# Optimization experiments

Hardware: AMD Instinct MI355X
Metric: run time of the kernel (lower is better)

Reference implementation:

```python
import jax, jax.numpy as jnp
import numpy as np

N_NODES = 100000
N_EDGES = 1600000
IN_F = 128
HID_F = 128
OUT_F = 128
HEAD_HID = 128
HEAD_OUT = 64


def setup_inputs() -> dict:
    key = jax.random.key(0)
    ks = jax.random.split(key, 16)
    glorot = lambda k, i, o: jax.random.normal(k, (i, o), jnp.float32) * (2.0 / (i + o)) ** 0.5
    return {
        "x": jax.random.normal(ks[0], (N_NODES, IN_F), jnp.float32),
        "src": jax.random.randint(ks[1], (N_EDGES,), 0, N_NODES),
        "dst": jax.random.randint(ks[2], (N_EDGES,), 0, N_NODES),
        "eps1": jnp.zeros((), jnp.float32),
        "eps2": jnp.zeros((), jnp.float32),
        # mlp_fun1: in_feats -> hid -> hid
        "w11": glorot(ks[3], IN_F, HID_F), "b11": jnp.zeros((HID_F,), jnp.float32),
        "w12": glorot(ks[4], HID_F, HID_F), "b12": jnp.zeros((HID_F,), jnp.float32),
        # mlp_fun2: hid -> hid -> out_feats
        "w21": glorot(ks[5], HID_F, HID_F), "b21": jnp.zeros((HID_F,), jnp.float32),
        "w22": glorot(ks[6], HID_F, OUT_F), "b22": jnp.zeros((OUT_F,), jnp.float32),
        # head mlp: out_feats -> hidden_dim -> output_dim (sigmoid)
        "wm1": glorot(ks[7], OUT_F, HEAD_HID), "bm1": jnp.zeros((HEAD_HID,), jnp.float32),
        "wm2": glorot(ks[8], HEAD_HID, HEAD_OUT), "bm2": jnp.zeros((HEAD_OUT,), jnp.float32),
    }


def _mlp2(h, w1, b1, w2, b2):
    # 2-layer MLP: Linear -> ReLU -> Linear
    return jax.nn.relu(h @ w1 + b1) @ w2 + b2


def _gin_conv(x, src, dst, eps, w1, b1, w2, b2):
    # sum-aggregate over incoming edges, then MLP update (DGL GINConv, learn_eps)
    agg = jax.ops.segment_sum(x[src], dst, num_segments=x.shape[0])  # [N, d]
    return _mlp2((1.0 + eps) * x + agg, w1, b1, w2, b2)


def reference(x, src, dst, eps1, eps2, w11, b11, w12, b12,
              w21, b21, w22, b22, wm1, bm1, wm2, bm2):
    # dropout is identity in eval mode
    h = jax.nn.relu(_gin_conv(x, src, dst, eps1, w11, b11, w12, b12))
    h = jax.nn.relu(_gin_conv(h, src, dst, eps2, w21, b21, w22, b22))
    # head MLP producing per-node probabilities (consumed by log-prob loss)
    return jax.nn.sigmoid(_mlp2(h, wm1, bm1, wm2, bm2))  # [N, output_dim]
```

## Files before the change

kernel.cpp:

```cpp
#include <hip/hip_runtime.h>

static constexpr int NN = 100000;
static constexpr int NE = 1600000;
static constexpr int NBUK = (NN + 255) / 256;
static constexpr int SC_BLOCKS = 400;
static constexpr int SC_CH = NE / SC_BLOCKS;

typedef float     f32x4  __attribute__((ext_vector_type(4)));
typedef _Float16  f16x8  __attribute__((ext_vector_type(8)));

static constexpr float LO_SCALE  = 16384.0f;
static constexpr float LO_USCALE = 1.0f / 16384.0f;

__device__ __forceinline__ unsigned pkh(float x, float y){
  unsigned short a = __builtin_bit_cast(unsigned short, (_Float16)x);
  unsigned short b = __builtin_bit_cast(unsigned short, (_Float16)y);
  return (unsigned)a | ((unsigned)b << 16);
}
__device__ __forceinline__ float2 uph(unsigned u){
  _Float16 a = __builtin_bit_cast(_Float16, (unsigned short)(u & 0xffffu));
  _Float16 b = __builtin_bit_cast(_Float16, (unsigned short)(u >> 16));
  return make_float2((float)a, (float)b);
}

__global__ void k_pack(const float* __restrict__ w11, const float* __restrict__ w12,
                       const float* __restrict__ w21, const float* __restrict__ w22,
                       const float* __restrict__ wm1, const float* __restrict__ wm2,
                       unsigned short* __restrict__ p11, unsigned short* __restrict__ p12,
                       unsigned short* __restrict__ p21, unsigned short* __restrict__ p22,
                       unsigned short* __restrict__ pm1, unsigned short* __restrict__ pm2){
  int b = blockIdx.x, lane = threadIdx.x;
  const float* W; unsigned short* P; int NCT, f;
  if (b < 160){
    int m = b >> 5; f = b & 31; NCT = 8;
    W = (m==0)?w11:(m==1)?w12:(m==2)?w21:(m==3)?w22:wm1;
    P = (m==0)?p11:(m==1)?p12:(m==2)?p21:(m==3)?p22:pm1;
  } else { f = b - 160; NCT = 4; W = wm2; P = pm2; }
  int NC = NCT * 16;
  int kt = f / NCT, ct = f % NCT;
  int hidx = ct >> 2, ct4 = ct & 3;
  int k0 = kt*32 + ((lane>>4)*8), col = ct*16 + (lane&15);
  unsigned short* dh = P + (hidx<<14) + ((kt*4+ct4)<<10) + (lane<<3);
  unsigned short* dl = dh + 512;
  #pragma unroll
  for (int j=0;j<8;j++){
    float v = W[(size_t)(k0+j)*NC + col];
    _Float16 h = (_Float16)v;
    _Float16 l = (_Float16)((v - (float)h) * LO_SCALE);
    dh[j] = __builtin_bit_cast(unsigned short, h);
    dl[j] = __builtin_bit_cast(unsigned short, l);
  }
}

__global__ void k_cvt(const float* __restrict__ x, unsigned* __restrict__ xh, int n4){
  int i = blockIdx.x*256 + threadIdx.x;
  if (i < n4){
    float4 v = reinterpret_cast<const float4*>(x)[i];
    uint2 o; o.x = pkh(v.x, v.y); o.y = pkh(v.z, v.w);
    reinterpret_cast<uint2*>(xh)[i] = o;
  }
}

__global__ __launch_bounds__(256) void k_hist(const int* __restrict__ dst, int* __restrict__ bhist){
  __shared__ int h[NBUK];
  int blk = blockIdx.x, t = threadIdx.x;
  for (int i=t;i<NBUK;i+=256) h[i]=0;
  __syncthreads();
  int e0 = blk*SC_CH;
  for (int e=e0+t; e<e0+SC_CH; e+=256) atomicAdd(&h[((unsigned)dst[e])>>8], 1);
  __syncthreads();
  for (int i=t;i<NBUK;i+=256){ int c=h[i]; if (c) atomicAdd(&bhist[i], c); }
}

__global__ void k_boff2(const int* __restrict__ bhist, int* __restrict__ boff){
  __shared__ int s[512];
  int t = threadIdx.x;
  int v = (t < NBUK) ? bhist[t] : 0;
  s[t] = v; __syncthreads();
  for (int off=1; off<512; off<<=1){
    int u = 0; if (t>=off) u = s[t-off];
    __syncthreads(); s[t] += u; __syncthreads();
  }
  if (t < NBUK) boff[t] = s[t] - v;
}

__global__ __launch_bounds__(256) void k_scatter1(const int* __restrict__ src,
                                                  const int* __restrict__ dst,
                                                  const int* __restrict__ boff,
                                                  int* __restrict__ gbcur,
                                                  uint2* __restrict__ tmp){
  __shared__ int hc[NBUK];
  __shared__ int hb[NBUK];
  int blk = blockIdx.x, t = threadIdx.x;
  int e0 = blk * SC_CH, e1 = e0 + SC_CH;
  for (int i=t;i<NBUK;i+=256) hc[i]=0;
  __syncthreads();
  for (int e=e0+t; e<e1; e+=256) atomicAdd(&hc[((unsigned)dst[e])>>8], 1);
  __syncthreads();
  for (int i=t;i<NBUK;i+=256){ int c = hc[i]; hb[i] = c ? atomicAdd(&gbcur[i], c) : 0; }
  __syncthreads();
  for (int i=t;i<NBUK;i+=256) hc[i]=0;
  __syncthreads();
  for (int e=e0+t; e<e1; e+=256){
    int d = dst[e]; int b = ((unsigned)d)>>8;
    int pos = atomicAdd(&hc[b], 1);
    tmp[(size_t)boff[b] + hb[b] + pos] = make_uint2((unsigned)src[e], (unsigned)d);
  }
}

__global__ __launch_bounds__(256) void k_fill2(const uint2* __restrict__ tmp,
                                               const int* __restrict__ boff,
                                               const int* __restrict__ bhist,
                                               int* __restrict__ eidx,
                                               int* __restrict__ rs, int* __restrict__ deg, int N){
  __shared__ int lh[256];
  __shared__ int ls[256];
  __shared__ int lc[256];
  int b = blockIdx.x, t = threadIdx.x;
  int base = boff[b], cnt = bhist[b];
  int nb0 = b*256;
  lh[t] = 0; lc[t] = 0;
  __syncthreads();
  for (int i=t; i<cnt; i+=256) atomicAdd(&lh[(int)tmp[(size_t)base+i].y - nb0], 1);
  __syncthreads();
  int v = lh[t];
  ls[t] = v; __syncthreads();
  for (int off=1; off<256; off<<=1){
    int u = 0; if (t>=off) u = ls[t-off];
    __syncthreads(); ls[t] += u; __syncthreads();
  }
  int node = nb0 + t;
  if (node < N){ deg[node] = v; rs[node] = base + ls[t] - v; }
  __syncthreads();
  for (int i=t; i<cnt; i+=256){
    uint2 e = tmp[(size_t)base+i];
    int local = (int)e.y - nb0;
    int pos = atomicAdd(&lc[local], 1);
    eidx[base + ls[local] - lh[local] + pos] = (int)e.x;
  }
}

__global__ __launch_bounds__(256) void k_agg(const unsigned* __restrict__ inp,
                                             unsigned* __restrict__ out,
                                             const float* __restrict__ epsp,
                                             const int* __restrict__ rs, const int* __restrict__ deg,
                                             const int* __restrict__ eidx, int N){
  int gw = (blockIdx.x*256 + threadIdx.x) >> 6;
  int lane = threadIdx.x & 63;
  if (gw >= N) return;
  float sc = 1.0f + *epsp;
  float2 v = uph(inp[(size_t)gw*64 + lane]);
  float a0 = sc * v.x, a1 = sc * v.y;
  int beg = rs[gw], d = deg[gw];
  int i = 0;
  for (; i+8 <= d; i += 8){
    unsigned u[8];
    #pragma unroll
    for (int j=0;j<8;j++) u[j] = inp[(size_t)eidx[beg+i+j]*64 + lane];
    #pragma unroll
    for (int j=0;j<8;j++){ float2 f = uph(u[j]); a0 += f.x; a1 += f.y; }
  }
  for (; i < d; ++i){
    float2 u = uph(inp[(size_t)eidx[beg+i]*64 + lane]);
    a0 += u.x; a1 += u.y;
  }
  out[(size_t)gw*64 + lane] = pkh(a0, a1);
}

static constexpr int HSTR = 136;
static constexpr int WSLICE = 32*HSTR;

__device__ __forceinline__ void load_a_glob2(const _Float16* __restrict__ t, int rbase,
                                             int lane, int N, f16x8 a[2][4]){
  #pragma unroll
  for (int ms=0; ms<2; ++ms){
    int row = rbase + ms*16 + (lane & 15); if (row >= N) row = N - 1;
    const _Float16* ap = t + (size_t)row*128 + ((lane>>4)*8);
    #pragma unroll
    for (int kt=0;kt<4;kt++) a[ms][kt] = *reinterpret_cast<const f16x8*>(ap + kt*32);
  }
}
__device__ __forceinline__ void load_a_lds2(const _Float16* slice, int lane, f16x8 a[2][4]){
  int ko = (lane>>4)*8;
  #pragma unroll
  for (int ms=0; ms<2; ++ms){
    const _Float16* rp = slice + (ms*16 + (lane&15))*HSTR + ko;
    #pragma unroll
    for (int kt=0;kt<4;kt++) a[ms][kt] = *reinterpret_cast<const f16x8*>(rp + kt*32);
  }
}

__device__ __forceinline__ void half_relu(const f16x8 a[2][4],
                                          const unsigned short* __restrict__ w,
                                          const float* __restrict__ bias,
                                          _Float16* slice, int lane, int hidx){
  const unsigned short* wb = w + (hidx<<14);
  int r0 = (lane>>4)*4, col0 = lane & 15;
  #pragma unroll
  for (int ct4=0; ct4<4; ++ct4){
    f32x4 c0={0.f,0.f,0.f,0.f}, c1={0.f,0.f,0.f,0.f};
    f32x4 d0={0.f,0.f,0.f,0.f}, d1={0.f,0.f,0.f,0.f};
    #pragma unroll
    for (int kt=0; kt<4; ++kt){
      const f16x8 bh = *reinterpret_cast<const f16x8*>(wb + ((kt*4+ct4)<<10) + (lane<<3));
      const f16x8 bl = *reinterpret_cast<const f16x8*>(wb + ((kt*4+ct4)<<10) + 512 + (lane<<3));
      c0 = __builtin_amdgcn_mfma_f32_16x16x32_f16(a[0][kt], bh, c0, 0,0,0);
      c1 = __builtin_amdgcn_mfma_f32_16x16x32_f16(a[1][kt], bh, c1, 0,0,0);
      d0 = __builtin_amdgcn_mfma_f32_16x16x32_f16(a[0][kt], bl, d0, 0,0,0);
      d1 = __builtin_amdgcn_mfma_f32_16x16x32_f16(a[1][kt], bl, d1, 0,0,0);
    }
    float bv = bias[hidx*64 + ct4*16 + col0];
    int cb = hidx*64 + ct4*16 + col0;
    #pragma unroll
    for (int r=0;r<4;r++){
      float v0 = fmaxf(c0[r] + d0[r]*LO_USCALE + bv, 0.f);
      float v1 = fmaxf(c1[r] + d1[r]*LO_USCALE + bv, 0.f);
      slice[(r0+r)*HSTR + cb]      = (_Float16)v0;
      slice[(16+r0+r)*HSTR + cb]   = (_Float16)v1;
    }
  }
}

__device__ __forceinline__ void head_sig(const f16x8 a[2][4],
                                         const unsigned short* __restrict__ w,
                                         const float* __restrict__ bias,
                                         float* fs, int lane){
  int r0 = (lane>>4)*4, col0 = lane & 15;
  #pragma unroll
  for (int ct4=0; ct4<4; ++ct4){
    f32x4 c0={0.f,0.f,0.f,0.f}, c1={0.f,0.f,0.f,0.f};
    f32x4 d0={0.f,0.f,0.f,0.f}, d1={0.f,0.f,0.f,0.f};
    #pragma unroll
    for (int kt=0; kt<4; ++kt){
      const f16x8 bh = *reinterpret_cast<const f16x8*>(w + ((kt*4+ct4)<<10) + (lane<<3));
      const f16x8 bl = *reinterpret_cast<const f16x8*>(w + ((kt*4+ct4)<<10) + 512 + (lane<<3));
      c0 = __builtin_amdgcn_mfma_f32_16x16x32_f16(a[0][kt], bh, c0, 0,0,0);
      c1 = __builtin_amdgcn_mfma_f32_16x16x32_f16(a[1][kt], bh, c1, 0,0,0);
      d0 = __builtin_amdgcn_mfma_f32_16x16x32_f16(a[0][kt], bl, d0, 0,0,0);
      d1 = __builtin_amdgcn_mfma_f32_16x16x32_f16(a[1][kt], bl, d1, 0,0,0);
    }
    float bv = bias[ct4*16 + col0];
    int cb = ct4*16 + col0;
    #pragma unroll
    for (int r=0;r<4;r++){
      float z0 = c0[r] + d0[r]*LO_USCALE + bv;
      float z1 = c1[r] + d1[r]*LO_USCALE + bv;
      fs[(r0+r)*68 + cb]    = 1.0f / (1.0f + __expf(-z0));
      fs[(16+r0+r)*68 + cb] = 1.0f / (1.0f + __expf(-z1));
    }
  }
}

__global__ __launch_bounds__(256) void k_mlp1(const _Float16* __restrict__ t,
    const unsigned short* __restrict__ w1, const float* __restrict__ b1,
    const unsigned short* __restrict__ w2, const float* __restrict__ b2,
    unsigned* __restrict__ h, int N){
  __shared__ _Float16 lds[4*WSLICE];
  int tid = threadIdx.x, lane = tid & 63, wv = tid >> 6;
  _Float16* slice = lds + wv*WSLICE;
  int rbase = blockIdx.x*128 + wv*32;
  f16x8 a[2][4];
  load_a_glob2(t, rbase, lane, N, a);
  half_relu(a, w1, b1, slice, lane, 0);
  half_relu(a, w1, b1, slice, lane, 1);
  load_a_lds2(slice, lane, a);
  half_relu(a, w2, b2, slice, lane, 0);
  half_relu(a, w2, b2, slice, lane, 1);
  for (int i=lane; i < 32*32; i += 64){
    int r = i >> 5, c = i & 31;
    if (rbase + r < N)
      reinterpret_cast<uint2*>(h)[(size_t)(rbase + r)*32 + c] =
        *reinterpret_cast<const uint2*>(slice + r*HSTR + c*4);
  }
}

__global__ __launch_bounds__(256) void k_mlp2_head(const _Float16* __restrict__ t,
    const unsigned short* __restrict__ w1, const float* __restrict__ b1,
    const unsigned short* __restrict__ w2, const float* __restrict__ b2,
    const unsigned short* __restrict__ w3, const float* __restrict__ b3,
    const unsigned short* __restrict__ w4, const float* __restrict__ b4,
    float* __restrict__ out, int N){
  __shared__ _Float16 lds[4*WSLICE];
  int tid = threadIdx.x, lane = tid & 63, wv = tid >> 6;
  _Float16* slice = lds + wv*WSLICE;
  int rbase = blockIdx.x*128 + wv*32;
  f16x8 a[2][4];
  load_a_glob2(t, rbase, lane, N, a);
  half_relu(a, w1, b1, slice, lane, 0);
  half_relu(a, w1, b1, slice, lane, 1);
  load_a_lds2(slice, lane, a);
  half_relu(a, w2, b2, slice, lane, 0);
  half_relu(a, w2, b2, slice, lane, 1);
  load_a_lds2(slice, lane, a);
  half_relu(a, w3, b3, slice, lane, 0);
  half_relu(a, w3, b3, slice, lane, 1);
  load_a_lds2(slice, lane, a);
  float* fs = reinterpret_cast<float*>(slice);
  head_sig(a, w4, b4, fs, lane);
  for (int i=lane; i < 32*16; i += 64){
    int r = i >> 4, c = i & 15;
    if (rbase + r < N)
      reinterpret_cast<float4*>(out)[(size_t)(rbase + r)*16 + c] =
        *reinterpret_cast<const float4*>(fs + r*68 + c*4);
  }
}

extern "C" void kernel_launch(void* const* d_in, const int* in_sizes, int n_in,
                              void* d_out, int out_size, void* d_ws, size_t ws_size,
                              hipStream_t stream) {
  const float* x   = (const float*)d_in[0];
  const int*   src = (const int*)  d_in[1];
  const int*   dst = (const int*)  d_in[2];
  const float* eps1= (const float*)d_in[3];
  const float* eps2= (const float*)d_in[4];
  const float* w11 = (const float*)d_in[5];  const float* b11 = (const float*)d_in[6];
  const float* w12 = (const float*)d_in[7];  const float* b12 = (const float*)d_in[8];
  const float* w21 = (const float*)d_in[9];  const float* b21 = (const float*)d_in[10];
  const float* w22 = (const float*)d_in[11]; const float* b22 = (const float*)d_in[12];
  const float* wm1 = (const float*)d_in[13]; const float* bm1 = (const float*)d_in[14];
  const float* wm2 = (const float*)d_in[15]; const float* bm2 = (const float*)d_in[16];

  char* ws = (char*)d_ws;
  size_t off = 0;
  auto alloc = [&](size_t bytes) -> void* {
    void* p = ws + off;
    off = (off + bytes + 255) & ~(size_t)255;
    return p;
  };
  unsigned* xh  = (unsigned*)alloc((size_t)NN*64*4);
  unsigned* B0  = (unsigned*)alloc((size_t)NN*64*4);
  unsigned* h1h = (unsigned*)alloc((size_t)NN*64*4);
  uint2* tmp = (uint2*)alloc((size_t)NE*8);
  int* eidx = (int*)alloc((size_t)NE*4);
  int* deg  = (int*)alloc((size_t)NN*4);
  int* rs   = (int*)alloc((size_t)NN*4);
  int* bhist= (int*)alloc((size_t)NBUK*4);
  int* boff = (int*)alloc((size_t)NBUK*4);
  int* gbcur= (int*)alloc((size_t)NBUK*4);
  unsigned short* p11 = (unsigned short*)alloc(128*128*2*2);
  unsigned short* p12 = (unsigned short*)alloc(128*128*2*2);
  unsigned short* p21 = (unsigned short*)alloc(128*128*2*2);
  unsigned short* p22 = (unsigned short*)alloc(128*128*2*2);
  unsigned short* pm1 = (unsigned short*)alloc(128*128*2*2);
  unsigned short* pm2 = (unsigned short*)alloc(128*64*2*2);
  if (off > ws_size) return;

  hipMemsetAsync(bhist, 0, (size_t)NBUK*4, stream);
  hipMemsetAsync(gbcur, 0, (size_t)NBUK*4, stream);

  k_pack<<<176, 64, 0, stream>>>(w11,w12,w21,w22,wm1,wm2, p11,p12,p21,p22,pm1,pm2);
  k_cvt<<<(NN*32 + 255)/256, 256, 0, stream>>>(x, xh, NN*32);
  k_hist<<<SC_BLOCKS, 256, 0, stream>>>(dst, bhist);
  k_boff2<<<1, 512, 0, stream>>>(bhist, boff);
  k_scatter1<<<SC_BLOCKS, 256, 0, stream>>>(src, dst, boff, gbcur, tmp);
  k_fill2<<<NBUK, 256, 0, stream>>>(tmp, boff, bhist, eidx, rs, deg, NN);

  int mgrid = (NN + 127) / 128;
  k_agg<<<(NN+3)/4, 256, 0, stream>>>(xh, B0, eps1, rs, deg, eidx, NN);
  k_mlp1<<<mgrid, 256, 0, stream>>>((const _Float16*)B0, p11, b11, p12, b12, h1h, NN);
  k_agg<<<(NN+3)/4, 256, 0, stream>>>(h1h, B0, eps2, rs, deg, eidx, NN);
  k_mlp2_head<<<mgrid, 256, 0, stream>>>((const _Float16*)B0, p21, b21, p22, b22,
                                         pm1, bm1, pm2, bm2, (float*)d_out, NN);
}
```

Baseline: 301.2 us.

## Pack edge bucket entries, widen buckets, unroll aggregation, use nontemporal stores

Destination buckets now span 1024 nodes instead of 256, and each scattered edge becomes a single 32-bit word holding the source index in the high bits and the local destination in the low 10 bits. This halves the temporary buffer traffic and cuts the number of fill blocks, with a two-level scan in the fill kernel. The aggregation kernel gains a 16-wide unrolled gather for more memory-level parallelism, and several output writes become nontemporal stores. Extra __syncthreads calls are added between MLP stages, which may add stalls. Packing the source as src<<10 assumes node ids fit in 22 bits.

```diff
diff --git a/kernel.cpp b/kernel.cpp
--- a/kernel.cpp
+++ b/kernel.cpp
@@ -2,12 +2,13 @@
 
 static constexpr int NN = 100000;
 static constexpr int NE = 1600000;
-static constexpr int NBUK = (NN + 255) / 256;
+static constexpr int NBUK = (NN + 1023) / 1024;
 static constexpr int SC_BLOCKS = 400;
 static constexpr int SC_CH = NE / SC_BLOCKS;
 
 typedef float     f32x4  __attribute__((ext_vector_type(4)));
 typedef _Float16  f16x8  __attribute__((ext_vector_type(8)));
+typedef unsigned  u32x2  __attribute__((ext_vector_type(2)));
 
 static constexpr float LO_SCALE  = 16384.0f;
 static constexpr float LO_USCALE = 1.0f / 16384.0f;
@@ -56,8 +57,9 @@
   int i = blockIdx.x*256 + threadIdx.x;
   if (i < n4){
     float4 v = reinterpret_cast<const float4*>(x)[i];
-    uint2 o; o.x = pkh(v.x, v.y); o.y = pkh(v.z, v.w);
-    reinterpret_cast<uint2*>(xh)[i] = o;
+    unsigned long long o = (unsigned long long)pkh(v.x, v.y)
+                         | ((unsigned long long)pkh(v.z, v.w) << 32);
+    __builtin_nontemporal_store(o, reinterpret_cast<unsigned long long*>(xh) + i);
   }
 }
 
@@ -67,17 +69,17 @@
   for (int i=t;i<NBUK;i+=256) h[i]=0;
   __syncthreads();
   int e0 = blk*SC_CH;
-  for (int e=e0+t; e<e0+SC_CH; e+=256) atomicAdd(&h[((unsigned)dst[e])>>8], 1);
+  for (int e=e0+t; e<e0+SC_CH; e+=256) atomicAdd(&h[((unsigned)dst[e])>>10], 1);
   __syncthreads();
   for (int i=t;i<NBUK;i+=256){ int c=h[i]; if (c) atomicAdd(&bhist[i], c); }
 }
 
 __global__ void k_boff2(const int* __restrict__ bhist, int* __restrict__ boff){
-  __shared__ int s[512];
+  __shared__ int s[128];
   int t = threadIdx.x;
   int v = (t < NBUK) ? bhist[t] : 0;
   s[t] = v; __syncthreads();
-  for (int off=1; off<512; off<<=1){
+  for (int off=1; off<128; off<<=1){
     int u = 0; if (t>=off) u = s[t-off];
     __syncthreads(); s[t] += u; __syncthreads();
   }
@@ -88,55 +90,65 @@
                                                   const int* __restrict__ dst,
                                                   const int* __restrict__ boff,
                                                   int* __restrict__ gbcur,
-                                                  uint2* __restrict__ tmp){
+                                                  unsigned* __restrict__ tmp){
   __shared__ int hc[NBUK];
   __shared__ int hb[NBUK];
   int blk = blockIdx.x, t = threadIdx.x;
   int e0 = blk * SC_CH, e1 = e0 + SC_CH;
   for (int i=t;i<NBUK;i+=256) hc[i]=0;
   __syncthreads();
-  for (int e=e0+t; e<e1; e+=256) atomicAdd(&hc[((unsigned)dst[e])>>8], 1);
+  for (int e=e0+t; e<e1; e+=256) atomicAdd(&hc[((unsigned)dst[e])>>10], 1);
   __syncthreads();
   for (int i=t;i<NBUK;i+=256){ int c = hc[i]; hb[i] = c ? atomicAdd(&gbcur[i], c) : 0; }
   __syncthreads();
   for (int i=t;i<NBUK;i+=256) hc[i]=0;
   __syncthreads();
   for (int e=e0+t; e<e1; e+=256){
-    int d = dst[e]; int b = ((unsigned)d)>>8;
+    unsigned d = (unsigned)dst[e]; unsigned b = d>>10;
     int pos = atomicAdd(&hc[b], 1);
-    tmp[(size_t)boff[b] + hb[b] + pos] = make_uint2((unsigned)src[e], (unsigned)d);
-  }
-}
-
-__global__ __launch_bounds__(256) void k_fill2(const uint2* __restrict__ tmp,
+    tmp[(size_t)boff[b] + hb[b] + pos] = ((unsigned)src[e] << 10) | (d & 1023u);
+  }
+}
+
+__global__ __launch_bounds__(256) void k_fill2(const unsigned* __restrict__ tmp,
                                                const int* __restrict__ boff,
                                                const int* __restrict__ bhist,
                                                int* __restrict__ eidx,
                                                int* __restrict__ rs, int* __restrict__ deg, int N){
-  __shared__ int lh[256];
-  __shared__ int ls[256];
-  __shared__ int lc[256];
+  __shared__ int lh[1024];
+  __shared__ int ls[1024];
+  __shared__ int lc[1024];
+  __shared__ int wsum[256];
   int b = blockIdx.x, t = threadIdx.x;
   int base = boff[b], cnt = bhist[b];
-  int nb0 = b*256;
-  lh[t] = 0; lc[t] = 0;
-  __syncthreads();
-  for (int i=t; i<cnt; i+=256) atomicAdd(&lh[(int)tmp[(size_t)base+i].y - nb0], 1);
-  __syncthreads();
-  int v = lh[t];
-  ls[t] = v; __syncthreads();
+  int nb0 = b*1024;
+  for (int i=t;i<1024;i+=256){ lh[i]=0; lc[i]=0; }
+  __syncthreads();
+  for (int i=t; i<cnt; i+=256) atomicAdd(&lh[tmp[(size_t)base+i] & 1023u], 1);
+  __syncthreads();
+  int v4[4]; int sum = 0;
+  #pragma unroll
+  for (int j=0;j<4;j++){ v4[j] = lh[t*4+j]; sum += v4[j]; }
+  wsum[t] = sum; __syncthreads();
   for (int off=1; off<256; off<<=1){
-    int u = 0; if (t>=off) u = ls[t-off];
-    __syncthreads(); ls[t] += u; __syncthreads();
-  }
-  int node = nb0 + t;
-  if (node < N){ deg[node] = v; rs[node] = base + ls[t] - v; }
+    int u = 0; if (t>=off) u = wsum[t-off];
+    __syncthreads(); wsum[t] += u; __syncthreads();
+  }
+  int run = wsum[t] - sum;
+  #pragma unroll
+  for (int j=0;j<4;j++){ ls[t*4+j] = run; run += v4[j]; }
+  __syncthreads();
+  #pragma unroll
+  for (int j=0;j<4;j++){
+    int node = nb0 + t*4 + j;
+    if (node < N){ deg[node] = v4[j]; rs[node] = base + ls[t*4+j]; }
+  }
   __syncthreads();
   for (int i=t; i<cnt; i+=256){
-    uint2 e = tmp[(size_t)base+i];
-    int local = (int)e.y - nb0;
+    unsigned e = tmp[(size_t)base+i];
+    int local = e & 1023u;
     int pos = atomicAdd(&lc[local], 1);
-    eidx[base + ls[local] - lh[local] + pos] = (int)e.x;
+    eidx[base + ls[local] + pos] = (int)(e >> 10);
   }
 }
 
@@ -153,6 +165,13 @@
   float a0 = sc * v.x, a1 = sc * v.y;
   int beg = rs[gw], d = deg[gw];
   int i = 0;
+  for (; i+16 <= d; i += 16){
+    unsigned u[16];
+    #pragma unroll
+    for (int j=0;j<16;j++) u[j] = inp[(size_t)eidx[beg+i+j]*64 + lane];
+    #pragma unroll
+    for (int j=0;j<16;j++){ float2 f = uph(u[j]); a0 += f.x; a1 += f.y; }
+  }
   for (; i+8 <= d; i += 8){
     unsigned u[8];
     #pragma unroll
@@ -164,7 +183,7 @@
     float2 u = uph(inp[(size_t)eidx[beg+i]*64 + lane]);
     a0 += u.x; a1 += u.y;
   }
-  out[(size_t)gw*64 + lane] = pkh(a0, a1);
+  __builtin_nontemporal_store(pkh(a0, a1), out + (size_t)gw*64 + lane);
 }
 
 static constexpr int HSTR = 136;
@@ -262,15 +281,20 @@
   f16x8 a[2][4];
   load_a_glob2(t, rbase, lane, N, a);
   half_relu(a, w1, b1, slice, lane, 0);
+  __syncthreads();
   half_relu(a, w1, b1, slice, lane, 1);
+  __syncthreads();
   load_a_lds2(slice, lane, a);
   half_relu(a, w2, b2, slice, lane, 0);
+  __syncthreads();
   half_relu(a, w2, b2, slice, lane, 1);
   for (int i=lane; i < 32*32; i += 64){
     int r = i >> 5, c = i & 31;
-    if (rbase + r < N)
-      reinterpret_cast<uint2*>(h)[(size_t)(rbase + r)*32 + c] =
-        *reinterpret_cast<const uint2*>(slice + r*HSTR + c*4);
+    if (rbase + r < N){
+      unsigned long long o = *reinterpret_cast<const unsigned long long*>(slice + r*HSTR + c*4);
+      __builtin_nontemporal_store(o,
+        reinterpret_cast<unsigned long long*>(h) + (size_t)(rbase + r)*32 + c);
+    }
   }
 }
 
@@ -287,21 +311,29 @@
   f16x8 a[2][4];
   load_a_glob2(t, rbase, lane, N, a);
   half_relu(a, w1, b1, slice, lane, 0);
+  __syncthreads();
   half_relu(a, w1, b1, slice, lane, 1);
+  __syncthreads();
   load_a_lds2(slice, lane, a);
   half_relu(a, w2, b2, slice, lane, 0);
+  __syncthreads();
   half_relu(a, w2, b2, slice, lane, 1);
+  __syncthreads();
   load_a_lds2(slice, lane, a);
   half_relu(a, w3, b3, slice, lane, 0);
+  __syncthreads();
   half_relu(a, w3, b3, slice, lane, 1);
+  __syncthreads();
   load_a_lds2(slice, lane, a);
   float* fs = reinterpret_cast<float*>(slice);
   head_sig(a, w4, b4, fs, lane);
   for (int i=lane; i < 32*16; i += 64){
     int r = i >> 4, c = i & 15;
-    if (rbase + r < N)
-      reinterpret_cast<float4*>(out)[(size_t)(rbase + r)*16 + c] =
-        *reinterpret_cast<const float4*>(fs + r*68 + c*4);
+    if (rbase + r < N){
+      f32x4 o = *reinterpret_cast<const f32x4*>(fs + r*68 + c*4);
+      __builtin_nontemporal_store(o,
+        reinterpret_cast<f32x4*>(out) + (size_t)(rbase + r)*16 + c);
+    }
   }
 }
 
@@ -330,7 +362,7 @@
   unsigned* xh  = (unsigned*)alloc((size_t)NN*64*4);
   unsigned* B0  = (unsigned*)alloc((size_t)NN*64*4);
   unsigned* h1h = (unsigned*)alloc((size_t)NN*64*4);
-  uint2* tmp = (uint2*)alloc((size_t)NE*8);
+  unsigned* tmp = (unsigned*)alloc((size_t)NE*4);
   int* eidx = (int*)alloc((size_t)NE*4);
   int* deg  = (int*)alloc((size_t)NN*4);
   int* rs   = (int*)alloc((size_t)NN*4);
@@ -351,7 +383,7 @@
   k_pack<<<176, 64, 0, stream>>>(w11,w12,w21,w22,wm1,wm2, p11,p12,p21,p22,pm1,pm2);
   k_cvt<<<(NN*32 + 255)/256, 256, 0, stream>>>(x, xh, NN*32);
   k_hist<<<SC_BLOCKS, 256, 0, stream>>>(dst, bhist);
-  k_boff2<<<1, 512, 0, stream>>>(bhist, boff);
+  k_boff2<<<1, 128, 0, stream>>>(bhist, boff);
   k_scatter1<<<SC_BLOCKS, 256, 0, stream>>>(src, dst, boff, gbcur, tmp);
   k_fill2<<<NBUK, 256, 0, stream>>>(tmp, boff, bhist, eidx, rs, deg, NN);
 
```

New measurement: 317.5 us. 5.4% more time.
